# Kernel tuning notes

Measured on AMD Instinct MI355X. Metric: run time of the kernel, lower is better.

The kernel has to match this reference:

```python
import jax, jax.numpy as jnp
import numpy as np

N_NODES = 50000
N_EDGES = 1600000
IN_CH = 128
HID = 32
HEADS = 4
N_LAYERS = 3
NEG_SLOPE = 0.2


def setup_inputs() -> dict:
    key = jax.random.key(0)
    ks = jax.random.split(key, 2 + 6 * N_LAYERS)
    inp = {
        "x": jax.random.normal(ks[0], (N_NODES, IN_CH), dtype=jnp.float32),
        "edge_index": jax.random.randint(ks[1], (2, N_EDGES), 0, N_NODES, dtype=jnp.int64),
    }
    HC = HID * HEADS  # 128, equals IN_CH so all layers share shapes
    for l in range(N_LAYERS):
        fan_in = IN_CH if l == 0 else HC
        s = 1.0 / np.sqrt(fan_in)
        k = ks[2 + 6 * l: 2 + 6 * (l + 1)]
        inp[f"Wl{l}"] = jax.random.normal(k[0], (fan_in, HC), dtype=jnp.float32) * s
        inp[f"bl{l}"] = jnp.zeros((HC,), dtype=jnp.float32)
        inp[f"Wr{l}"] = jax.random.normal(k[1], (fan_in, HC), dtype=jnp.float32) * s
        inp[f"br{l}"] = jnp.zeros((HC,), dtype=jnp.float32)
        inp[f"att{l}"] = jax.random.normal(k[2], (HEADS, HID), dtype=jnp.float32) * (1.0 / np.sqrt(HID))
        inp[f"b{l}"] = jnp.zeros((HC,), dtype=jnp.float32)
    return inp


def gatv2_layer(x, src, dst, Wl, bl, Wr, br, att, b):
    # GATv2Conv: xl = lin_l(x) for source msgs, xr = lin_r(x) for targets
    xl = (x @ Wl + bl).reshape(N_NODES, HEADS, HID)
    xr = (x @ Wr + br).reshape(N_NODES, HEADS, HID)
    h = xl[src] + xr[dst]                                   # [E, H, C] gather
    e = jnp.sum(att * jax.nn.leaky_relu(h, NEG_SLOPE), -1)  # [E, H] per-edge score
    # segment softmax over incoming edges of each dst node
    m = jax.ops.segment_max(e, dst, num_segments=N_NODES)   # [N, H]
    w = jnp.exp(e - m[dst])
    z = jax.ops.segment_sum(w, dst, num_segments=N_NODES)
    alpha = w / z[dst]                                      # [E, H]
    out = jax.ops.segment_sum(alpha[..., None] * xl[src], dst, num_segments=N_NODES)
    return out.reshape(N_NODES, HEADS * HID) + b


def reference(x, edge_index, Wl0, bl0, Wr0, br0, att0, b0,
              Wl1, bl1, Wr1, br1, att1, b1,
              Wl2, bl2, Wr2, br2, att2, b2):
    # add self loops (PyG GATv2Conv default add_self_loops=True)
    loops = jnp.arange(N_NODES, dtype=edge_index.dtype)
    src = jnp.concatenate([edge_index[0], loops])
    dst = jnp.concatenate([edge_index[1], loops])
    params = [(Wl0, bl0, Wr0, br0, att0, b0),
              (Wl1, bl1, Wr1, br1, att1, b1),
              (Wl2, bl2, Wr2, br2, att2, b2)]
    for i, p in enumerate(params):
        x = gatv2_layer(x, src, dst, *p)
        if i < N_LAYERS - 1:
            x = jax.nn.elu(x)  # dropout p=0.0 / eval mode -> identity
    return x
```

## Files before the change

### kernel.cpp

```cpp
#include <hip/hip_runtime.h>
#include <hip/hip_fp16.h>
#include <math.h>

#define N_NODES 50000
#define N_EDGES 1600000
#define ETOT (N_EDGES + N_NODES)
#define HC 128
#define HEADS 4
#define HID 32
#define NEG_SLOPE 0.2f
#define NPB 32
#define NBUCKETS ((N_NODES + NPB - 1) / NPB)
#define CHUNK 8192
#define NCHUNK ((ETOT + CHUNK - 1) / CHUNK)
#define LOG2E 1.4426950408889634f
#define NEGBIG (-1e30f)

typedef _Float16 h2 __attribute__((ext_vector_type(2)));

__device__ __forceinline__ unsigned pack2(float a, float b) {
    return ((unsigned)__half_as_ushort(__float2half(b)) << 16) | __half_as_ushort(__float2half(a));
}

__device__ __forceinline__ float fdot2u(unsigned a, unsigned b, float c) {
#if __has_builtin(__builtin_amdgcn_fdot2)
    return __builtin_amdgcn_fdot2(__builtin_bit_cast(h2, a), __builtin_bit_cast(h2, b), c, false);
#else
    h2 ha = __builtin_bit_cast(h2, a);
    h2 hb = __builtin_bit_cast(h2, b);
    return fmaf((float)ha[0], (float)hb[0], fmaf((float)ha[1], (float)hb[1], c));
#endif
}


__global__ __launch_bounds__(256) void hist_kernel(const int* __restrict__ dstArr, int* __restrict__ deg) {
    int i = blockIdx.x * 256 + threadIdx.x;
    if (i >= ETOT) return;
    int d = (i < N_EDGES) ? dstArr[i] : (i - N_EDGES);
    atomicAdd(&deg[d], 1);
}

__global__ __launch_bounds__(1024) void scanA_kernel(const int* __restrict__ deg,
                                                     int* __restrict__ rowStart, int* __restrict__ blockSum) {
    __shared__ int buf[1024];
    int i = blockIdx.x * 1024 + threadIdx.x;
    int v = (i < N_NODES) ? deg[i] : 0;
    buf[threadIdx.x] = v;
    __syncthreads();
    for (int off = 1; off < 1024; off <<= 1) {
        int t = (threadIdx.x >= off) ? buf[threadIdx.x - off] : 0;
        __syncthreads();
        buf[threadIdx.x] += t;
        __syncthreads();
    }
    if (i < N_NODES) rowStart[i] = buf[threadIdx.x] - v;
    if (threadIdx.x == 1023) blockSum[blockIdx.x] = buf[1023];
}

__global__ void scanB_kernel(const int* __restrict__ blockSum, int* __restrict__ blockOff, int nb) {
    if (threadIdx.x == 0 && blockIdx.x == 0) {
        int acc = 0;
        for (int j = 0; j < nb; j++) { blockOff[j] = acc; acc += blockSum[j]; }
    }
}

__global__ __launch_bounds__(1024) void scanC_kernel(int* __restrict__ rowStart, const int* __restrict__ blockOff,
                                                     int* __restrict__ bucketCursor) {
    int i = blockIdx.x * 1024 + threadIdx.x;
    if (i < N_NODES) {
        int v = rowStart[i] + blockOff[blockIdx.x];
        rowStart[i] = v;
        if ((i & (NPB - 1)) == 0) bucketCursor[i >> 5] = v;
    }
    if (i == 0) rowStart[N_NODES] = ETOT;
}

__global__ __launch_bounds__(256) void chunk_scatter_kernel(const int* __restrict__ srcArr, const int* __restrict__ dstArr,
                                                            int* __restrict__ bucketCursor, int* __restrict__ E) {
    __shared__ int hist[NBUCKETS];
    int c0 = blockIdx.x * CHUNK;
    int c1 = min(c0 + CHUNK, ETOT);
    for (int b = threadIdx.x; b < NBUCKETS; b += 256) hist[b] = 0;
    __syncthreads();

    int myP[CHUNK / 256];
    int cnt = 0;
    for (int i = c0 + threadIdx.x; i < c1; i += 256) {
        int s, d;
        if (i < N_EDGES) { s = srcArr[i]; d = dstArr[i]; }
        else             { s = i - N_EDGES; d = s; }
        myP[cnt] = s | (d << 16);
        cnt++;
        atomicAdd(&hist[d >> 5], 1);
    }
    __syncthreads();
    for (int b = threadIdx.x; b < NBUCKETS; b += 256) {
        int h = hist[b];
        hist[b] = (h > 0) ? atomicAdd(&bucketCursor[b], h) : 0;
    }
    __syncthreads();
    for (int k = 0; k < cnt; k++) {
        int pe = myP[k];
        int pos = atomicAdd(&hist[((unsigned)pe) >> 21], 1);
        E[pos] = pe;
    }
}

__global__ __launch_bounds__(256) void csr_scatter_kernel(const int* __restrict__ E, const int* __restrict__ rowStart,
                                                          int* __restrict__ srcOff) {
    __shared__ int lcur[NPB];
    int b = blockIdx.x;
    int n0 = b * NPB;
    int nend = min(n0 + NPB, N_NODES);
    if (threadIdx.x < nend - n0) lcur[threadIdx.x] = rowStart[n0 + threadIdx.x];
    __syncthreads();
    int e0 = rowStart[n0];
    int e1 = rowStart[nend];
    for (int i = e0 + threadIdx.x; i < e1; i += 256) {
        int pe = E[i];
        int pos = atomicAdd(&lcur[(pe >> 16) & (NPB - 1)], 1);
        srcOff[pos] = (pe & 0xFFFF) << 8;
    }
}


__global__ __launch_bounds__(256) void cvt_x_kernel(const float* __restrict__ x, __half* __restrict__ xh) {
    int i = blockIdx.x * 256 + threadIdx.x;
    if (i >= N_NODES * HC / 8) return;
    const float4* s = reinterpret_cast<const float4*>(x + (size_t)i * 8);
    float4 v0 = s[0], v1 = s[1];
    uint4 o;
    o.x = pack2(v0.x, v0.y); o.y = pack2(v0.z, v0.w);
    o.z = pack2(v1.x, v1.y); o.w = pack2(v1.z, v1.w);
    reinterpret_cast<uint4*>(xh)[i] = o;
}

__global__ __launch_bounds__(256) void pack_w_kernel(const float* __restrict__ Wl, const float* __restrict__ Wr,
                                                     unsigned* __restrict__ Wp) {
    int i = blockIdx.x * 256 + threadIdx.x;
    if (i >= 2 * 64 * HC) return;
    int mat = i >> 13;
    int k2 = (i >> 7) & 63;
    int n = i & 127;
    const float* W = mat ? Wr : Wl;
    Wp[i] = pack2(W[(2 * k2) * HC + n], W[(2 * k2 + 1) * HC + n]);
}


__global__ __launch_bounds__(256) void gemm_kernel(const __half* __restrict__ xin,
    const unsigned* __restrict__ Wp, const float* __restrict__ bl, const float* __restrict__ br,
    __half* __restrict__ XLh, float* __restrict__ XR) {
    __shared__ unsigned As2[128][20];
    __shared__ unsigned Bs2[16][132];
    int t = threadIdx.x;
    int rb = blockIdx.x * 128;
    int mat = blockIdx.y;
    const float* bias = mat ? br : bl;
    int tx = t & 15, ty = t >> 4;

    float acc00[4][4], acc01[4][4], acc10[4][4], acc11[4][4];
#pragma unroll
    for (int i = 0; i < 4; i++)
#pragma unroll
        for (int j = 0; j < 4; j++) { acc00[i][j] = 0.f; acc01[i][j] = 0.f; acc10[i][j] = 0.f; acc11[i][j] = 0.f; }

    for (int kt = 0; kt < 4; kt++) {
#pragma unroll
        for (int it = 0; it < 2; it++) {
            int idx = it * 256 + t;
            int r = idx >> 2, f = idx & 3;
            int gr = rb + r;
            uint4 v = make_uint4(0, 0, 0, 0);
            if (gr < N_NODES) v = *reinterpret_cast<const uint4*>(xin + (size_t)gr * HC + kt * 32 + f * 8);
            *reinterpret_cast<uint4*>(&As2[r][f * 4]) = v;
        }
#pragma unroll
        for (int it = 0; it < 2; it++) {
            int idx = it * 256 + t;
            int k2 = idx >> 5, f = idx & 31;
            *reinterpret_cast<uint4*>(&Bs2[k2][f * 4]) =
                *reinterpret_cast<const uint4*>(Wp + ((size_t)(mat * 64 + kt * 16 + k2) * HC + f * 4));
        }
        __syncthreads();
#pragma unroll
        for (int k2 = 0; k2 < 16; k2++) {
            uint4 bv0 = *reinterpret_cast<const uint4*>(&Bs2[k2][tx * 4]);
            uint4 bv1 = *reinterpret_cast<const uint4*>(&Bs2[k2][64 + tx * 4]);
            unsigned av[8];
#pragma unroll
            for (int i = 0; i < 4; i++) av[i] = As2[ty * 4 + i][k2];
#pragma unroll
            for (int i = 0; i < 4; i++) av[4 + i] = As2[64 + ty * 4 + i][k2];
#pragma unroll
            for (int i = 0; i < 4; i++) {
                acc00[i][0] = fdot2u(av[i], bv0.x, acc00[i][0]);
                acc00[i][1] = fdot2u(av[i], bv0.y, acc00[i][1]);
                acc00[i][2] = fdot2u(av[i], bv0.z, acc00[i][2]);
                acc00[i][3] = fdot2u(av[i], bv0.w, acc00[i][3]);
                acc01[i][0] = fdot2u(av[i], bv1.x, acc01[i][0]);
                acc01[i][1] = fdot2u(av[i], bv1.y, acc01[i][1]);
                acc01[i][2] = fdot2u(av[i], bv1.z, acc01[i][2]);
                acc01[i][3] = fdot2u(av[i], bv1.w, acc01[i][3]);
                acc10[i][0] = fdot2u(av[4 + i], bv0.x, acc10[i][0]);
                acc10[i][1] = fdot2u(av[4 + i], bv0.y, acc10[i][1]);
                acc10[i][2] = fdot2u(av[4 + i], bv0.z, acc10[i][2]);
                acc10[i][3] = fdot2u(av[4 + i], bv0.w, acc10[i][3]);
                acc11[i][0] = fdot2u(av[4 + i], bv1.x, acc11[i][0]);
                acc11[i][1] = fdot2u(av[4 + i], bv1.y, acc11[i][1]);
                acc11[i][2] = fdot2u(av[4 + i], bv1.z, acc11[i][2]);
                acc11[i][3] = fdot2u(av[4 + i], bv1.w, acc11[i][3]);
            }
        }
        __syncthreads();
    }

    float4 bb0 = *reinterpret_cast<const float4*>(&bias[tx * 4]);
    float4 bb1 = *reinterpret_cast<const float4*>(&bias[64 + tx * 4]);
#pragma unroll
    for (int i = 0; i < 4; i++) {
        int gr0 = rb + ty * 4 + i;
        int gr1 = rb + 64 + ty * 4 + i;
        float4 o00, o01, o10, o11;
        o00.x = acc00[i][0] + bb0.x; o00.y = acc00[i][1] + bb0.y; o00.z = acc00[i][2] + bb0.z; o00.w = acc00[i][3] + bb0.w;
        o01.x = acc01[i][0] + bb1.x; o01.y = acc01[i][1] + bb1.y; o01.z = acc01[i][2] + bb1.z; o01.w = acc01[i][3] + bb1.w;
        o10.x = acc10[i][0] + bb0.x; o10.y = acc10[i][1] + bb0.y; o10.z = acc10[i][2] + bb0.z; o10.w = acc10[i][3] + bb0.w;
        o11.x = acc11[i][0] + bb1.x; o11.y = acc11[i][1] + bb1.y; o11.z = acc11[i][2] + bb1.z; o11.w = acc11[i][3] + bb1.w;
        if (mat == 0) {
            if (gr0 < N_NODES) {
                uint2 u0, u1;
                u0.x = pack2(o00.x, o00.y); u0.y = pack2(o00.z, o00.w);
                u1.x = pack2(o01.x, o01.y); u1.y = pack2(o01.z, o01.w);
                *reinterpret_cast<uint2*>(&XLh[(size_t)gr0 * HC + tx * 4]) = u0;
                *reinterpret_cast<uint2*>(&XLh[(size_t)gr0 * HC + 64 + tx * 4]) = u1;
            }
            if (gr1 < N_NODES) {
                uint2 u0, u1;
                u0.x = pack2(o10.x, o10.y); u0.y = pack2(o10.z, o10.w);
                u1.x = pack2(o11.x, o11.y); u1.y = pack2(o11.z, o11.w);
                *reinterpret_cast<uint2*>(&XLh[(size_t)gr1 * HC + tx * 4]) = u0;
                *reinterpret_cast<uint2*>(&XLh[(size_t)gr1 * HC + 64 + tx * 4]) = u1;
            }
        } else {
            if (gr0 < N_NODES) {
                *reinterpret_cast<float4*>(&XR[(size_t)gr0 * HC + tx * 4]) = o00;
                *reinterpret_cast<float4*>(&XR[(size_t)gr0 * HC + 64 + tx * 4]) = o01;
            }
            if (gr1 < N_NODES) {
                *reinterpret_cast<float4*>(&XR[(size_t)gr1 * HC + tx * 4]) = o10;
                *reinterpret_cast<float4*>(&XR[(size_t)gr1 * HC + 64 + tx * 4]) = o11;
            }
        }
    }
}


__device__ __forceinline__ float score8p(uint4 xl, const unsigned* __restrict__ xrh,
                                         const unsigned* __restrict__ ah) {
    const h2 slope = { (_Float16)NEG_SLOPE, (_Float16)NEG_SLOPE };
    unsigned u[4] = { xl.x, xl.y, xl.z, xl.w };
    float c = 0.f;
#pragma unroll
    for (int j = 0; j < 4; j++) {
        h2 s = __builtin_bit_cast(h2, u[j]) + __builtin_bit_cast(h2, xrh[j]);
        h2 t = s * slope;
        h2 m = __builtin_elementwise_max(s, t);
        c = fdot2u(__builtin_bit_cast(unsigned, m), ah[j], c);
    }
    c += __shfl_xor(c, 1);
    c += __shfl_xor(c, 2);
    return fminf(c, 120.f);
}

__device__ __forceinline__ void upd8p(float c, uint4 xl, float& z, float* __restrict__ acc) {
    float w = exp2f(c);
    z += w;
    unsigned u[4] = { xl.x, xl.y, xl.z, xl.w };
#pragma unroll
    for (int j = 0; j < 4; j++) {
        h2 h = __builtin_bit_cast(h2, u[j]);
        acc[2 * j]     = fmaf(w, (float)h[0], acc[2 * j]);
        acc[2 * j + 1] = fmaf(w, (float)h[1], acc[2 * j + 1]);
    }
}

__global__ __launch_bounds__(256) void gat_fused_kernel(const __half* __restrict__ XLh,
    const float* __restrict__ XR, const float* __restrict__ att,
    const int* __restrict__ rowStart, const int* __restrict__ srcOff,
    const float* __restrict__ bvec, float* __restrict__ outF, __half* __restrict__ outH,
    int applyElu) {
    int wv = threadIdx.x >> 6;
    int l = threadIdx.x & 63;
    int q = l >> 4;
    int cl = l & 15;
    int n = blockIdx.x * 4 + wv;
    if (n >= N_NODES) return;
    int s0 = rowStart[n], s1 = rowStart[n + 1];

    unsigned xrh[4], ah[4];
    {
        float4 x0 = *reinterpret_cast<const float4*>(&XR[(size_t)n * HC + 8 * cl]);
        float4 x1 = *reinterpret_cast<const float4*>(&XR[(size_t)n * HC + 8 * cl + 4]);
        float4 a0 = *reinterpret_cast<const float4*>(&att[8 * cl]);
        float4 a1 = *reinterpret_cast<const float4*>(&att[8 * cl + 4]);
        xrh[0] = pack2(x0.x, x0.y); xrh[1] = pack2(x0.z, x0.w);
        xrh[2] = pack2(x1.x, x1.y); xrh[3] = pack2(x1.z, x1.w);
        ah[0] = pack2(a0.x * LOG2E, a0.y * LOG2E); ah[1] = pack2(a0.z * LOG2E, a0.w * LOG2E);
        ah[2] = pack2(a1.x * LOG2E, a1.y * LOG2E); ah[3] = pack2(a1.z * LOG2E, a1.w * LOG2E);
    }
    const char* XLb = reinterpret_cast<const char*>(XLh) + 16 * cl;

    float z = 0.f;
    float acc[8];
#pragma unroll
    for (int i = 0; i < 8; i++) acc[i] = 0.f;

    int p = s0;
    for (; p + 16 <= s1; p += 16) {
        int oA = srcOff[p      + q];
        int oB = srcOff[p + 4  + q];
        int oC = srcOff[p + 8  + q];
        int oD = srcOff[p + 12 + q];
        uint4 xA = *reinterpret_cast<const uint4*>(XLb + (size_t)(unsigned)oA);
        uint4 xB = *reinterpret_cast<const uint4*>(XLb + (size_t)(unsigned)oB);
        uint4 xC = *reinterpret_cast<const uint4*>(XLb + (size_t)(unsigned)oC);
        uint4 xD = *reinterpret_cast<const uint4*>(XLb + (size_t)(unsigned)oD);
        float cA = score8p(xA, xrh, ah);
        float cB = score8p(xB, xrh, ah);
        float cC = score8p(xC, xrh, ah);
        float cD = score8p(xD, xrh, ah);
        upd8p(cA, xA, z, acc);
        upd8p(cB, xB, z, acc);
        upd8p(cC, xC, z, acc);
        upd8p(cD, xD, z, acc);
    }
    for (; p + 4 <= s1; p += 4) {
        int o = srcOff[p + q];
        uint4 x = *reinterpret_cast<const uint4*>(XLb + (size_t)(unsigned)o);
        float c = score8p(x, xrh, ah);
        upd8p(c, x, z, acc);
    }
    if (p < s1) {
        int r = s1 - p;
        int o = srcOff[min(p + q, s1 - 1)];
        uint4 x = *reinterpret_cast<const uint4*>(XLb + (size_t)(unsigned)o);
        float c = score8p(x, xrh, ah);
        if (q >= r) c = NEGBIG;
        upd8p(c, x, z, acc);
    }

    z += __shfl_xor(z, 16);
    z += __shfl_xor(z, 32);
#pragma unroll
    for (int i = 0; i < 8; i++) {
        acc[i] += __shfl_xor(acc[i], 16);
        acc[i] += __shfl_xor(acc[i], 32);
    }

    if (q == 0) {
        float zinv = 1.f / z;
        float4 b0 = *reinterpret_cast<const float4*>(&bvec[8 * cl]);
        float4 b1 = *reinterpret_cast<const float4*>(&bvec[8 * cl + 4]);
        float o0[8];
        o0[0] = acc[0] * zinv + b0.x; o0[1] = acc[1] * zinv + b0.y;
        o0[2] = acc[2] * zinv + b0.z; o0[3] = acc[3] * zinv + b0.w;
        o0[4] = acc[4] * zinv + b1.x; o0[5] = acc[5] * zinv + b1.y;
        o0[6] = acc[6] * zinv + b1.z; o0[7] = acc[7] * zinv + b1.w;
        if (applyElu) {
#pragma unroll
            for (int i = 0; i < 8; i++) o0[i] = o0[i] > 0.f ? o0[i] : (__expf(o0[i]) - 1.f);
        }
        if (outH) {
            uint4 u;
            u.x = pack2(o0[0], o0[1]); u.y = pack2(o0[2], o0[3]);
            u.z = pack2(o0[4], o0[5]); u.w = pack2(o0[6], o0[7]);
            *reinterpret_cast<uint4*>(&outH[(size_t)n * HC + 8 * cl]) = u;
        } else {
            *reinterpret_cast<float4*>(&outF[(size_t)n * HC + 8 * cl]) = make_float4(o0[0], o0[1], o0[2], o0[3]);
            *reinterpret_cast<float4*>(&outF[(size_t)n * HC + 8 * cl + 4]) = make_float4(o0[4], o0[5], o0[6], o0[7]);
        }
    }
}


extern "C" void kernel_launch(void* const* d_in, const int* in_sizes, int n_in,
                              void* d_out, int out_size, void* d_ws, size_t ws_size,
                              hipStream_t stream) {
    const float* x = (const float*)d_in[0];
    const int* ei = (const int*)d_in[1];
    const int* srcArr = ei;
    const int* dstArr = ei + N_EDGES;

    char* ws = (char*)d_ws;
    size_t off = 0;
    auto alloc = [&](size_t bytes) -> void* {
        void* p = ws + off;
        off = (off + bytes + 511) & ~(size_t)511;
        return p;
    };
    __half* xh     = (__half*)alloc((size_t)N_NODES * HC * 2);
    __half* Ph     = (__half*)alloc((size_t)N_NODES * HC * 2);
    __half* XLh    = (__half*)alloc((size_t)N_NODES * HC * 2);
    float* XR      = (float*)alloc((size_t)N_NODES * HC * 4);
    unsigned* Wp   = (unsigned*)alloc((size_t)2 * 64 * HC * 4);
    int* deg       = (int*)alloc((size_t)N_NODES * 4);
    int* rowStart  = (int*)alloc((size_t)(N_NODES + 1) * 4);
    int* blockSum  = (int*)alloc(64 * 4);
    int* blockOff  = (int*)alloc(64 * 4);
    int* bucketCur = (int*)alloc((size_t)NBUCKETS * 4);
    int* E         = (int*)alloc((size_t)ETOT * 4);
    int* srcOff    = (int*)alloc((size_t)ETOT * 4);

    const int NSCAN = (N_NODES + 1023) / 1024;

    (void)hipMemsetAsync(deg, 0, (size_t)N_NODES * 4, stream);
    hist_kernel<<<(ETOT + 255) / 256, 256, 0, stream>>>(dstArr, deg);
    scanA_kernel<<<NSCAN, 1024, 0, stream>>>(deg, rowStart, blockSum);
    scanB_kernel<<<1, 64, 0, stream>>>(blockSum, blockOff, NSCAN);
    scanC_kernel<<<NSCAN, 1024, 0, stream>>>(rowStart, blockOff, bucketCur);
    chunk_scatter_kernel<<<NCHUNK, 256, 0, stream>>>(srcArr, dstArr, bucketCur, E);
    csr_scatter_kernel<<<NBUCKETS, 256, 0, stream>>>(E, rowStart, srcOff);
    cvt_x_kernel<<<(N_NODES * HC / 8 + 255) / 256, 256, 0, stream>>>(x, xh);

    for (int lyr = 0; lyr < 3; lyr++) {
        const __half* gin = (lyr == 0) ? xh : Ph;
        const float* Wl  = (const float*)d_in[2 + 6 * lyr + 0];
        const float* bl  = (const float*)d_in[2 + 6 * lyr + 1];
        const float* Wr  = (const float*)d_in[2 + 6 * lyr + 2];
        const float* br  = (const float*)d_in[2 + 6 * lyr + 3];
        const float* att = (const float*)d_in[2 + 6 * lyr + 4];
        const float* bb  = (const float*)d_in[2 + 6 * lyr + 5];

        pack_w_kernel<<<(2 * 64 * HC + 255) / 256, 256, 0, stream>>>(Wl, Wr, Wp);

        dim3 ggrid((N_NODES + 127) / 128, 2);
        gemm_kernel<<<ggrid, 256, 0, stream>>>(gin, Wp, bl, br, XLh, XR);

        int nb = (N_NODES + 3) / 4;
        gat_fused_kernel<<<nb, 256, 0, stream>>>(XLh, XR, att, rowStart, srcOff, bb,
                                                 lyr == 2 ? (float*)d_out : nullptr,
                                                 lyr < 2 ? Ph : nullptr,
                                                 lyr < 2 ? 1 : 0);
    }
}
```

Measured before the change: 430.6 us.

## Build CSR via bucket histogram and derive row starts inside bucket scatter

Replaces the per-node global-atomic degree histogram and three-kernel scan with a per-chunk shared-memory bucket histogram, followed by a single-block scan over the buckets. Per-node row starts are now computed inside csr_scatter by counting each bucket's edges in shared memory. This cuts global atomics and removes two kernel launches. In exchange, csr_scatter reads E twice, and the scan runs serially in one block over about 1563 buckets.

```diff
diff --git a/kernel.cpp b/kernel.cpp
--- a/kernel.cpp
+++ b/kernel.cpp
@@ -33,46 +33,56 @@
 }
 
 
-__global__ __launch_bounds__(256) void hist_kernel(const int* __restrict__ dstArr, int* __restrict__ deg) {
-    int i = blockIdx.x * 256 + threadIdx.x;
-    if (i >= ETOT) return;
-    int d = (i < N_EDGES) ? dstArr[i] : (i - N_EDGES);
-    atomicAdd(&deg[d], 1);
-}
-
-__global__ __launch_bounds__(1024) void scanA_kernel(const int* __restrict__ deg,
-                                                     int* __restrict__ rowStart, int* __restrict__ blockSum) {
+__global__ __launch_bounds__(256) void bucket_hist_kernel(const int* __restrict__ dstArr,
+                                                          int* __restrict__ bucketCount) {
+    __shared__ int hist[NBUCKETS];
+    int c0 = blockIdx.x * CHUNK;
+    int c1 = min(c0 + CHUNK, ETOT);
+    for (int b = threadIdx.x; b < NBUCKETS; b += 256) hist[b] = 0;
+    __syncthreads();
+    for (int i = c0 + threadIdx.x; i < c1; i += 256) {
+        int d = (i < N_EDGES) ? dstArr[i] : (i - N_EDGES);
+        atomicAdd(&hist[d >> 5], 1);
+    }
+    __syncthreads();
+    for (int b = threadIdx.x; b < NBUCKETS; b += 256) {
+        int h = hist[b];
+        if (h > 0) atomicAdd(&bucketCount[b], h);
+    }
+}
+
+__global__ __launch_bounds__(1024) void bucket_scan_kernel(const int* __restrict__ bucketCount,
+                                                           int* __restrict__ bucketStart,
+                                                           int* __restrict__ bucketCursor,
+                                                           int* __restrict__ rowStart) {
     __shared__ int buf[1024];
-    int i = blockIdx.x * 1024 + threadIdx.x;
-    int v = (i < N_NODES) ? deg[i] : 0;
-    buf[threadIdx.x] = v;
-    __syncthreads();
-    for (int off = 1; off < 1024; off <<= 1) {
-        int t = (threadIdx.x >= off) ? buf[threadIdx.x - off] : 0;
+    __shared__ int carry;
+    if (threadIdx.x == 0) carry = 0;
+    __syncthreads();
+    for (int base = 0; base < NBUCKETS; base += 1024) {
+        int i = base + threadIdx.x;
+        int v = (i < NBUCKETS) ? bucketCount[i] : 0;
+        buf[threadIdx.x] = v;
         __syncthreads();
-        buf[threadIdx.x] += t;
+        for (int off = 1; off < 1024; off <<= 1) {
+            int t = (threadIdx.x >= off) ? buf[threadIdx.x - off] : 0;
+            __syncthreads();
+            buf[threadIdx.x] += t;
+            __syncthreads();
+        }
+        if (i < NBUCKETS) {
+            int excl = carry + buf[threadIdx.x] - v;
+            bucketStart[i] = excl;
+            bucketCursor[i] = excl;
+        }
         __syncthreads();
-    }
-    if (i < N_NODES) rowStart[i] = buf[threadIdx.x] - v;
-    if (threadIdx.x == 1023) blockSum[blockIdx.x] = buf[1023];
-}
-
-__global__ void scanB_kernel(const int* __restrict__ blockSum, int* __restrict__ blockOff, int nb) {
-    if (threadIdx.x == 0 && blockIdx.x == 0) {
-        int acc = 0;
-        for (int j = 0; j < nb; j++) { blockOff[j] = acc; acc += blockSum[j]; }
-    }
-}
-
-__global__ __launch_bounds__(1024) void scanC_kernel(int* __restrict__ rowStart, const int* __restrict__ blockOff,
-                                                     int* __restrict__ bucketCursor) {
-    int i = blockIdx.x * 1024 + threadIdx.x;
-    if (i < N_NODES) {
-        int v = rowStart[i] + blockOff[blockIdx.x];
-        rowStart[i] = v;
-        if ((i & (NPB - 1)) == 0) bucketCursor[i >> 5] = v;
-    }
-    if (i == 0) rowStart[N_NODES] = ETOT;
+        if (threadIdx.x == 1023) carry += buf[1023];
+        __syncthreads();
+    }
+    if (threadIdx.x == 0) {
+        bucketStart[NBUCKETS] = ETOT;
+        rowStart[N_NODES] = ETOT;
+    }
 }
 
 __global__ __launch_bounds__(256) void chunk_scatter_kernel(const int* __restrict__ srcArr, const int* __restrict__ dstArr,
@@ -106,16 +116,32 @@
     }
 }
 
-__global__ __launch_bounds__(256) void csr_scatter_kernel(const int* __restrict__ E, const int* __restrict__ rowStart,
+__global__ __launch_bounds__(256) void csr_scatter_kernel(const int* __restrict__ E,
+                                                          const int* __restrict__ bucketStart,
+                                                          int* __restrict__ rowStart,
                                                           int* __restrict__ srcOff) {
+    __shared__ int cnt[NPB];
     __shared__ int lcur[NPB];
     int b = blockIdx.x;
     int n0 = b * NPB;
-    int nend = min(n0 + NPB, N_NODES);
-    if (threadIdx.x < nend - n0) lcur[threadIdx.x] = rowStart[n0 + threadIdx.x];
-    __syncthreads();
-    int e0 = rowStart[n0];
-    int e1 = rowStart[nend];
+    int e0 = bucketStart[b];
+    int e1 = bucketStart[b + 1];
+    if (threadIdx.x < NPB) cnt[threadIdx.x] = 0;
+    __syncthreads();
+    for (int i = e0 + threadIdx.x; i < e1; i += 256)
+        atomicAdd(&cnt[(E[i] >> 16) & (NPB - 1)], 1);
+    __syncthreads();
+    if (threadIdx.x == 0) {
+        int run = e0;
+#pragma unroll
+        for (int j = 0; j < NPB; j++) {
+            lcur[j] = run;
+            int n = n0 + j;
+            if (n < N_NODES) rowStart[n] = run;
+            run += cnt[j];
+        }
+    }
+    __syncthreads();
     for (int i = e0 + threadIdx.x; i < e1; i += 256) {
         int pe = E[i];
         int pos = atomicAdd(&lcur[(pe >> 16) & (NPB - 1)], 1);
@@ -397,28 +423,23 @@
         off = (off + bytes + 511) & ~(size_t)511;
         return p;
     };
-    __half* xh     = (__half*)alloc((size_t)N_NODES * HC * 2);
-    __half* Ph     = (__half*)alloc((size_t)N_NODES * HC * 2);
-    __half* XLh    = (__half*)alloc((size_t)N_NODES * HC * 2);
-    float* XR      = (float*)alloc((size_t)N_NODES * HC * 4);
-    unsigned* Wp   = (unsigned*)alloc((size_t)2 * 64 * HC * 4);
-    int* deg       = (int*)alloc((size_t)N_NODES * 4);
-    int* rowStart  = (int*)alloc((size_t)(N_NODES + 1) * 4);
-    int* blockSum  = (int*)alloc(64 * 4);
-    int* blockOff  = (int*)alloc(64 * 4);
-    int* bucketCur = (int*)alloc((size_t)NBUCKETS * 4);
-    int* E         = (int*)alloc((size_t)ETOT * 4);
-    int* srcOff    = (int*)alloc((size_t)ETOT * 4);
-
-    const int NSCAN = (N_NODES + 1023) / 1024;
-
-    (void)hipMemsetAsync(deg, 0, (size_t)N_NODES * 4, stream);
-    hist_kernel<<<(ETOT + 255) / 256, 256, 0, stream>>>(dstArr, deg);
-    scanA_kernel<<<NSCAN, 1024, 0, stream>>>(deg, rowStart, blockSum);
-    scanB_kernel<<<1, 64, 0, stream>>>(blockSum, blockOff, NSCAN);
-    scanC_kernel<<<NSCAN, 1024, 0, stream>>>(rowStart, blockOff, bucketCur);
+    __half* xh      = (__half*)alloc((size_t)N_NODES * HC * 2);
+    __half* Ph      = (__half*)alloc((size_t)N_NODES * HC * 2);
+    __half* XLh     = (__half*)alloc((size_t)N_NODES * HC * 2);
+    float* XR       = (float*)alloc((size_t)N_NODES * HC * 4);
+    unsigned* Wp    = (unsigned*)alloc((size_t)2 * 64 * HC * 4);
+    int* rowStart   = (int*)alloc((size_t)(N_NODES + 1) * 4);
+    int* bucketCnt  = (int*)alloc((size_t)NBUCKETS * 4);
+    int* bucketStart= (int*)alloc((size_t)(NBUCKETS + 1) * 4);
+    int* bucketCur  = (int*)alloc((size_t)NBUCKETS * 4);
+    int* E          = (int*)alloc((size_t)ETOT * 4);
+    int* srcOff     = (int*)alloc((size_t)ETOT * 4);
+
+    (void)hipMemsetAsync(bucketCnt, 0, (size_t)NBUCKETS * 4, stream);
+    bucket_hist_kernel<<<NCHUNK, 256, 0, stream>>>(dstArr, bucketCnt);
+    bucket_scan_kernel<<<1, 1024, 0, stream>>>(bucketCnt, bucketStart, bucketCur, rowStart);
     chunk_scatter_kernel<<<NCHUNK, 256, 0, stream>>>(srcArr, dstArr, bucketCur, E);
-    csr_scatter_kernel<<<NBUCKETS, 256, 0, stream>>>(E, rowStart, srcOff);
+    csr_scatter_kernel<<<NBUCKETS, 256, 0, stream>>>(E, bucketStart, rowStart, srcOff);
     cvt_x_kernel<<<(N_NODES * HC / 8 + 255) / 256, 256, 0, stream>>>(x, xh);
 
     for (int lyr = 0; lyr < 3; lyr++) {
```

Result: faster. 374.2 us (-13.1%).
